# Performance work log

Measured on AMD Instinct MI355X. Metric: run time of the kernel, lower is better.

The kernel has to match this reference:

```python
import jax, jax.numpy as jnp
import numpy as np


def setup_inputs() -> dict:
    key = jax.random.key(0)
    k1, k2, k3 = jax.random.split(key, 3)
    n1, n2, L, n_S, sub_dim = 768, 768, 128, 30, 16
    X1 = jax.random.randint(k1, (n1, L), 0, n_S, dtype=jnp.int64)
    X2 = jax.random.randint(k2, (n2, L), 0, n_S, dtype=jnp.int64)
    a = jnp.ones((1,), dtype=jnp.float32)  # Parameter a=1.0
    A = jax.random.normal(k3, (n_S, sub_dim), dtype=jnp.float32)  # nn.init.normal_(A, 0, 1)
    w_vec = jnp.zeros((L * (L - 1) // 2,), dtype=jnp.float32)  # torch.zeros init
    return {"X1": X1, "X2": X2, "a": a, "A": A, "w_vec": w_vec}


def reference(X1, X2, a, A, w_vec):
    n1, L = X1.shape
    n2, _ = X2.shape
    # build symmetric soft weight matrix; diagonal stays sigmoid(0)=0.5 as in torch
    i_x, i_y = np.tril_indices(L, k=-1)
    W = jnp.zeros((L, L), dtype=w_vec.dtype)
    W = W.at[i_x, i_y].set(w_vec).at[i_y, i_x].set(w_vec)
    w = jax.nn.sigmoid(W)  # (L, L)

    S = A @ A.T  # (n_S, n_S) substitution matrix

    def wdk(subs):
        # quadratic form sum_{i,j} subs[...,i] * w[i,j] * subs[...,j]
        return jnp.sum((subs @ w) * subs, axis=-1)

    d1 = S[X1, X1]            # (n1, L) self-substitution scores
    d2 = S[X2, X2]            # (n2, L)
    k1 = wdk(d1)[:, None]     # (n1, 1)
    k2 = wdk(d2)[None, :]     # (1, n2)

    # cross pair gather: subs[a, b, l] = S[X1[a, l], X2[b, l]]  -> (n1, n2, L)
    subs = S[X1[:, None, :], X2[None, :, :]]
    K = wdk(subs)             # (n1, n2)

    K = K / jnp.sqrt(k1) / jnp.sqrt(k2)
    return a ** 2 * K
```

## Files before the change

kernel.cpp:

```cpp
#include <hip/hip_runtime.h>
#include <hip/hip_bf16.h>

typedef __attribute__((ext_vector_type(8))) short short8;
typedef __attribute__((ext_vector_type(4))) float f32x4;
typedef unsigned long long ull;

#define N1 768
#define N2 768
#define LL 128
#define NS 30

__device__ __forceinline__ unsigned short f2b(float f) {
  unsigned int u = __float_as_uint(f);
  unsigned int r = (u + 0x7fffu + ((u >> 16) & 1u)) >> 16;
  return (unsigned short)r;
}

__global__ void prep_kernel(const float* __restrict__ A, const float* __restrict__ w_vec,
                            float* __restrict__ wf, unsigned short* __restrict__ wb,
                            float* __restrict__ Sdiag, unsigned short* __restrict__ Sbg) {
  int b = blockIdx.x, t = threadIdx.x;
  if (b == 0) {
    for (int idx = t; idx < NS * NS; idx += 256) {
      int i = idx / NS, j = idx - i * NS;
      float acc = 0.f;
#pragma unroll
      for (int k = 0; k < 16; ++k) acc += A[i * 16 + k] * A[j * 16 + k];
      Sbg[i * 32 + j] = f2b(acc);
      if (i == j) Sdiag[i] = acc;
    }
  } else {
    int base = (b - 1) * 512;
#pragma unroll
    for (int k = 0; k < 2; ++k) {
      int idx = base + k * 256 + t;
      int l = idx >> 7, mm = idx & (LL - 1);
      float sig;
      if (l == mm) {
        sig = 0.5f;
      } else {
        int hi = l > mm ? l : mm, lo = l > mm ? mm : l;
        sig = 1.f / (1.f + expf(-w_vec[hi * (hi - 1) / 2 + lo]));
      }
      wf[idx] = sig;
      wb[idx] = f2b(sig);
    }
  }
}

__global__ __launch_bounds__(128) void norm_kernel(
    const int* __restrict__ X1, const int* __restrict__ X2,
    const float* __restrict__ Sdiag, const float* __restrict__ wf,
    float* __restrict__ inv1, float* __restrict__ inv2,
    const float* __restrict__ a_ptr) {
  __shared__ __align__(16) float d[8][LL];
  __shared__ float wsum[2][8];
  const int t = threadIdx.x;
  const int r0 = blockIdx.x * 8;
#pragma unroll
  for (int r = 0; r < 8; ++r) {
    int row = r0 + r;
    const int* X = (row < N1) ? (X1 + row * LL) : (X2 + (row - N1) * LL);
    d[r][t] = Sdiag[X[t]];
  }
  __syncthreads();
  const float4* w4 = reinterpret_cast<const float4*>(wf + t * LL);
  float s[8] = {0.f, 0.f, 0.f, 0.f, 0.f, 0.f, 0.f, 0.f};
#pragma unroll 8
  for (int q = 0; q < 32; ++q) {
    float4 wv = w4[q];
#pragma unroll
    for (int r = 0; r < 8; ++r) {
      float4 dd = *reinterpret_cast<const float4*>(&d[r][q * 4]);
      s[r] += wv.x * dd.x + wv.y * dd.y + wv.z * dd.z + wv.w * dd.w;
    }
  }
#pragma unroll
  for (int r = 0; r < 8; ++r) {
    float v = s[r] * d[r][t];
    v += __shfl_xor(v, 1);
    v += __shfl_xor(v, 2);
    v += __shfl_xor(v, 4);
    v += __shfl_xor(v, 8);
    v += __shfl_xor(v, 16);
    v += __shfl_xor(v, 32);
    if ((t & 63) == 0) wsum[t >> 6][r] = v;
  }
  __syncthreads();
  if (t < 8) {
    int row = r0 + t;
    float k = wsum[0][t] + wsum[1][t];
    if (row < N1) inv1[row] = a_ptr[0] * a_ptr[0] / sqrtf(k);
    else inv2[row - N1] = 1.f / sqrtf(k);
  }
}

__global__ __launch_bounds__(512, 4) void main_kernel(
    const int* __restrict__ X1, const int* __restrict__ X2,
    const unsigned short* __restrict__ wbg, const unsigned short* __restrict__ Sbg,
    const float* __restrict__ inv1, const float* __restrict__ inv2,
    float* __restrict__ out) {
  __shared__ __align__(16) unsigned short sV[256 * LL];
  __shared__ __align__(16) unsigned short sSb[960];
  __shared__ __align__(16) unsigned char x1B[16 * 144];
  __shared__ __align__(16) unsigned char x2B[16 * 144];
  __shared__ __align__(16) float red[4 * 256];

  const int t = threadIdx.x;
  const int lane = t & 63, wave = t >> 6;
  const int m = lane & 15, kg = lane >> 4;
  const int i0 = blockIdx.y * 16, j0 = blockIdx.x * 16;
  char* sVb = reinterpret_cast<char*>(sV);

  float iv1v = 0.f, iv2v = 0.f;
  if (t < 256) {
    iv1v = inv1[i0 + (t >> 4)];
    iv2v = inv2[j0 + (t & 15)];
  }

  if (t < 120) reinterpret_cast<uint4*>(sSb)[t] = reinterpret_cast<const uint4*>(Sbg)[t];

  if (t < 256) {
    int row = t >> 4, seg = t & 15;
    const int4* p1 = reinterpret_cast<const int4*>(X1 + (i0 + row) * LL + seg * 8);
    int4 a0 = p1[0], a1 = p1[1];
    ull v = 0;
    v |= (ull)(a0.x & 0xff);
    v |= (ull)(a0.y & 0xff) << 8;
    v |= (ull)(a0.z & 0xff) << 16;
    v |= (ull)(a0.w & 0xff) << 24;
    v |= (ull)(a1.x & 0xff) << 32;
    v |= (ull)(a1.y & 0xff) << 40;
    v |= (ull)(a1.z & 0xff) << 48;
    v |= (ull)(a1.w & 0xff) << 56;
    *reinterpret_cast<ull*>(x1B + row * 144 + seg * 8) = v;
    const int4* p2p = reinterpret_cast<const int4*>(X2 + (j0 + row) * LL + seg * 8);
    int4 b0 = p2p[0], b1 = p2p[1];
    ull u = 0;
    u |= (ull)(b0.x & 0xff);
    u |= (ull)(b0.y & 0xff) << 8;
    u |= (ull)(b0.z & 0xff) << 16;
    u |= (ull)(b0.w & 0xff) << 24;
    u |= (ull)(b1.x & 0xff) << 32;
    u |= (ull)(b1.y & 0xff) << 40;
    u |= (ull)(b1.z & 0xff) << 48;
    u |= (ull)(b1.w & 0xff) << 56;
    *reinterpret_cast<ull*>(x2B + row * 144 + seg * 8) = u;
  }
  __syncthreads();

  {
    const int p2 = t & 255;
    const int h2 = t >> 8;
    const char* a1p = reinterpret_cast<const char*>(x1B) + (p2 >> 4) * 144 + 64 * h2;
    const char* a2p = reinterpret_cast<const char*>(x2B) + (p2 & 15) * 144 + 64 * h2;
    uint4 A0 = *reinterpret_cast<const uint4*>(a1p);
    uint4 A1 = *reinterpret_cast<const uint4*>(a1p + 16);
    uint4 A2 = *reinterpret_cast<const uint4*>(a1p + 32);
    uint4 A3 = *reinterpret_cast<const uint4*>(a1p + 48);
    uint4 B0 = *reinterpret_cast<const uint4*>(a2p);
    uint4 B1 = *reinterpret_cast<const uint4*>(a2p + 16);
    uint4 B2 = *reinterpret_cast<const uint4*>(a2p + 32);
    uint4 B3 = *reinterpret_cast<const uint4*>(a2p + 48);
    const int swz = (p2 & 7) << 4;
    char* wbase = sVb + p2 * 256;
#define QUAD(u1, u2, w0, w1)                                                        \
    {                                                                               \
      unsigned a0_ = (u1) & 255u, a1_ = ((u1) >> 8) & 255u;                         \
      unsigned a2_ = ((u1) >> 16) & 255u, a3_ = (u1) >> 24;                         \
      unsigned b0_ = (u2) & 255u, b1_ = ((u2) >> 8) & 255u;                         \
      unsigned b2_ = ((u2) >> 16) & 255u, b3_ = (u2) >> 24;                         \
      unsigned g0 = sSb[(a0_ << 5) | b0_];                                          \
      unsigned g1 = sSb[(a1_ << 5) | b1_];                                          \
      unsigned g2 = sSb[(a2_ << 5) | b2_];                                          \
      unsigned g3 = sSb[(a3_ << 5) | b3_];                                          \
      w0 = g0 | (g1 << 16);                                                         \
      w1 = g2 | (g3 << 16);                                                         \
    }
#define OCT(o, U1a, U2a, U1b, U2b)                                                  \
    {                                                                               \
      uint4 pk;                                                                     \
      QUAD(U1a, U2a, pk.x, pk.y)                                                    \
      QUAD(U1b, U2b, pk.z, pk.w)                                                    \
      *reinterpret_cast<uint4*>(wbase + ((128 * h2 + 16 * (o)) ^ swz)) = pk;        \
    }
    OCT(0, A0.x, B0.x, A0.y, B0.y)
    OCT(1, A0.z, B0.z, A0.w, B0.w)
    OCT(2, A1.x, B1.x, A1.y, B1.y)
    OCT(3, A1.z, B1.z, A1.w, B1.w)
    OCT(4, A2.x, B2.x, A2.y, B2.y)
    OCT(5, A2.z, B2.z, A2.w, B2.w)
    OCT(6, A3.x, B3.x, A3.y, B3.y)
    OCT(7, A3.z, B3.z, A3.w, B3.w)
#undef OCT
#undef QUAD
  }

  const int lg = wave & 3, ph = wave >> 2;
  short8 wreg[2][4];
  {
    const char* wby = reinterpret_cast<const char*>(wbg);
#pragma unroll
    for (int lt = 0; lt < 2; ++lt)
#pragma unroll
      for (int kk = 0; kk < 4; ++kk)
        wreg[lt][kk] = *reinterpret_cast<const short8*>(
            wby + (lg * 32 + lt * 16 + m) * 256 + kk * 64 + kg * 16);
  }
  __syncthreads();

#pragma unroll
  for (int pt = 0; pt < 8; ++pt) {
    const int p = ph * 128 + pt * 16 + m;
    const int sw = (p & 7) << 4;
    const char* base = sVb + p * 256;
    short8 bv[4];
#pragma unroll
    for (int kk = 0; kk < 4; ++kk)
      bv[kk] = *reinterpret_cast<const short8*>(base + ((kk * 64 + kg * 16) ^ sw));
    f32x4 a0 = {0.f, 0.f, 0.f, 0.f}, a1 = {0.f, 0.f, 0.f, 0.f};
#pragma unroll
    for (int kk = 0; kk < 4; ++kk) {
      a0 = __builtin_amdgcn_mfma_f32_16x16x32_bf16(wreg[0][kk], bv[kk], a0, 0, 0, 0);
      a1 = __builtin_amdgcn_mfma_f32_16x16x32_bf16(wreg[1][kk], bv[kk], a1, 0, 0, 0);
    }
    float kp = 0.f;
    {
      uint2 vv = *reinterpret_cast<const uint2*>(base + ((64 * lg + 8 * kg) ^ sw));
      kp += a0[0] * __uint_as_float(vv.x << 16) + a0[1] * __uint_as_float(vv.x & 0xffff0000u) +
            a0[2] * __uint_as_float(vv.y << 16) + a0[3] * __uint_as_float(vv.y & 0xffff0000u);
    }
    {
      uint2 vv = *reinterpret_cast<const uint2*>(base + ((64 * lg + 32 + 8 * kg) ^ sw));
      kp += a1[0] * __uint_as_float(vv.x << 16) + a1[1] * __uint_as_float(vv.x & 0xffff0000u) +
            a1[2] * __uint_as_float(vv.y << 16) + a1[3] * __uint_as_float(vv.y & 0xffff0000u);
    }
    kp += __shfl_xor(kp, 16);
    kp += __shfl_xor(kp, 32);
    if (kg == 0) red[lg * 256 + p] = kp;
  }
  __syncthreads();

  if (t < 256) {
    float s = red[t] + red[256 + t] + red[512 + t] + red[768 + t];
    out[(i0 + (t >> 4)) * N2 + j0 + (t & 15)] = s * iv1v * iv2v;
  }
}

extern "C" void kernel_launch(void* const* d_in, const int* in_sizes, int n_in,
                              void* d_out, int out_size, void* d_ws, size_t ws_size,
                              hipStream_t stream) {
  const int* X1 = (const int*)d_in[0];
  const int* X2 = (const int*)d_in[1];
  const float* a = (const float*)d_in[2];
  const float* A = (const float*)d_in[3];
  const float* w_vec = (const float*)d_in[4];
  float* out = (float*)d_out;

  char* ws = (char*)d_ws;
  float* wf = (float*)(ws + 0);
  unsigned short* wb = (unsigned short*)(ws + 65536);
  float* Sdiag = (float*)(ws + 98304);
  unsigned short* Sbg = (unsigned short*)(ws + 98432);
  float* inv1 = (float*)(ws + 100352);
  float* inv2 = (float*)(ws + 103424);

  prep_kernel<<<33, 256, 0, stream>>>(A, w_vec, wf, wb, Sdiag, Sbg);
  norm_kernel<<<(N1 + N2) / 8, 128, 0, stream>>>(X1, X2, Sdiag, wf, inv1, inv2, a);
  main_kernel<<<dim3(N2 / 16, N1 / 16), 512, 0, stream>>>(X1, X2, wb, Sbg, inv1, inv2, out);
}
```

Before: 54.22 us.

## Split MFMA work across waves by 64-row W slices instead of 32

Re-partitions the per-block quadratic-form work so each wave owns 64 rows of W (four 16-row tiles) and half the pairs, instead of 32 rows and all 128-pair halves. Each B fragment loaded from LDS is reused across four MFMA chains instead of two, which halves the LDS B reads and the reduction buffer size. W fragments are now loaded with inline-asm global loads followed by an explicit wait. The cost is double the W register footprint (16 short8 per lane), which may pressure VGPRs under the 512x4 launch bound.

```diff
diff --git a/kernel.cpp b/kernel.cpp
--- a/kernel.cpp
+++ b/kernel.cpp
@@ -104,7 +104,7 @@
   __shared__ __align__(16) unsigned short sSb[960];
   __shared__ __align__(16) unsigned char x1B[16 * 144];
   __shared__ __align__(16) unsigned char x2B[16 * 144];
-  __shared__ __align__(16) float red[4 * 256];
+  __shared__ __align__(16) float red[2 * 256];
 
   const int t = threadIdx.x;
   const int lane = t & 63, wave = t >> 6;
@@ -196,53 +196,53 @@
 #undef QUAD
   }
 
-  const int lg = wave & 3, ph = wave >> 2;
-  short8 wreg[2][4];
+  const int lg2 = wave & 1, ph = wave >> 1;
+  short8 wreg[4][4];
   {
-    const char* wby = reinterpret_cast<const char*>(wbg);
-#pragma unroll
-    for (int lt = 0; lt < 2; ++lt)
-#pragma unroll
-      for (int kk = 0; kk < 4; ++kk)
-        wreg[lt][kk] = *reinterpret_cast<const short8*>(
-            wby + (lg * 32 + lt * 16 + m) * 256 + kk * 64 + kg * 16);
-  }
-  __syncthreads();
-
-#pragma unroll
-  for (int pt = 0; pt < 8; ++pt) {
-    const int p = ph * 128 + pt * 16 + m;
+    const char* wby = reinterpret_cast<const char*>(wbg) + (lg2 * 64 + m) * 256 + kg * 16;
+#pragma unroll
+    for (int lt = 0; lt < 4; ++lt)
+#pragma unroll
+      for (int kk = 0; kk < 4; ++kk) {
+        const char* addr = wby + lt * 16 * 256 + kk * 64;
+        asm volatile("global_load_dwordx4 %0, %1, off"
+                     : "=v"(wreg[lt][kk])
+                     : "v"(addr));
+      }
+    asm volatile("s_waitcnt vmcnt(0)" ::: "memory");
+    __builtin_amdgcn_sched_barrier(0);
+  }
+  __syncthreads();
+
+#pragma unroll
+  for (int pt = 0; pt < 4; ++pt) {
+    const int p = ph * 64 + pt * 16 + m;
     const int sw = (p & 7) << 4;
     const char* base = sVb + p * 256;
     short8 bv[4];
 #pragma unroll
     for (int kk = 0; kk < 4; ++kk)
       bv[kk] = *reinterpret_cast<const short8*>(base + ((kk * 64 + kg * 16) ^ sw));
-    f32x4 a0 = {0.f, 0.f, 0.f, 0.f}, a1 = {0.f, 0.f, 0.f, 0.f};
-#pragma unroll
-    for (int kk = 0; kk < 4; ++kk) {
-      a0 = __builtin_amdgcn_mfma_f32_16x16x32_bf16(wreg[0][kk], bv[kk], a0, 0, 0, 0);
-      a1 = __builtin_amdgcn_mfma_f32_16x16x32_bf16(wreg[1][kk], bv[kk], a1, 0, 0, 0);
-    }
     float kp = 0.f;
-    {
-      uint2 vv = *reinterpret_cast<const uint2*>(base + ((64 * lg + 8 * kg) ^ sw));
-      kp += a0[0] * __uint_as_float(vv.x << 16) + a0[1] * __uint_as_float(vv.x & 0xffff0000u) +
-            a0[2] * __uint_as_float(vv.y << 16) + a0[3] * __uint_as_float(vv.y & 0xffff0000u);
-    }
-    {
-      uint2 vv = *reinterpret_cast<const uint2*>(base + ((64 * lg + 32 + 8 * kg) ^ sw));
-      kp += a1[0] * __uint_as_float(vv.x << 16) + a1[1] * __uint_as_float(vv.x & 0xffff0000u) +
-            a1[2] * __uint_as_float(vv.y << 16) + a1[3] * __uint_as_float(vv.y & 0xffff0000u);
+#pragma unroll
+    for (int lt = 0; lt < 4; ++lt) {
+      f32x4 acc = {0.f, 0.f, 0.f, 0.f};
+#pragma unroll
+      for (int kk = 0; kk < 4; ++kk)
+        acc = __builtin_amdgcn_mfma_f32_16x16x32_bf16(wreg[lt][kk], bv[kk], acc, 0, 0, 0);
+      uint2 vv = *reinterpret_cast<const uint2*>(
+          base + ((128 * lg2 + 32 * lt + 8 * kg) ^ sw));
+      kp += acc[0] * __uint_as_float(vv.x << 16) + acc[1] * __uint_as_float(vv.x & 0xffff0000u) +
+            acc[2] * __uint_as_float(vv.y << 16) + acc[3] * __uint_as_float(vv.y & 0xffff0000u);
     }
     kp += __shfl_xor(kp, 16);
     kp += __shfl_xor(kp, 32);
-    if (kg == 0) red[lg * 256 + p] = kp;
+    if (kg == 0) red[lg2 * 256 + p] = kp;
   }
   __syncthreads();
 
   if (t < 256) {
-    float s = red[t] + red[256 + t] + red[512 + t] + red[768 + t];
+    float s = red[t] + red[256 + t];
     out[(i0 + (t >> 4)) * N2 + j0 + (t & 15)] = s * iv1v * iv2v;
   }
 }
```

After: 73.63 us. +35.8%, slower.

## Merge prep and norm kernels into one launch, rebuild weights per block

Applied to the files above, without the earlier changes.

The separate prep and norm kernels are folded into a single aux kernel. The first 33 blocks write the bf16 weights and substitution matrix, and the remaining 192 blocks each recompute the sigmoid weight matrix and the self-substitution diagonal in shared memory to get the norms. This removes one kernel launch and the dependency between them, at the cost of redundant sigmoid and exp work per block and a serial loop of up to 127 iterations per thread with an unbalanced triangular workload. It also raises the wave priority around the MFMA loop in the main kernel.

```diff
diff --git a/kernel.cpp b/kernel.cpp
--- a/kernel.cpp
+++ b/kernel.cpp
@@ -16,80 +16,104 @@
   return (unsigned short)r;
 }
 
-__global__ void prep_kernel(const float* __restrict__ A, const float* __restrict__ w_vec,
-                            float* __restrict__ wf, unsigned short* __restrict__ wb,
-                            float* __restrict__ Sdiag, unsigned short* __restrict__ Sbg) {
-  int b = blockIdx.x, t = threadIdx.x;
-  if (b == 0) {
-    for (int idx = t; idx < NS * NS; idx += 256) {
-      int i = idx / NS, j = idx - i * NS;
-      float acc = 0.f;
-#pragma unroll
-      for (int k = 0; k < 16; ++k) acc += A[i * 16 + k] * A[j * 16 + k];
-      Sbg[i * 32 + j] = f2b(acc);
-      if (i == j) Sdiag[i] = acc;
-    }
-  } else {
-    int base = (b - 1) * 512;
-#pragma unroll
-    for (int k = 0; k < 2; ++k) {
-      int idx = base + k * 256 + t;
-      int l = idx >> 7, mm = idx & (LL - 1);
-      float sig;
-      if (l == mm) {
-        sig = 0.5f;
-      } else {
-        int hi = l > mm ? l : mm, lo = l > mm ? mm : l;
-        sig = 1.f / (1.f + expf(-w_vec[hi * (hi - 1) / 2 + lo]));
+__global__ __launch_bounds__(256) void aux_kernel(
+    const int* __restrict__ X1, const int* __restrict__ X2,
+    const float* __restrict__ A, const float* __restrict__ w_vec,
+    const float* __restrict__ a_ptr, unsigned short* __restrict__ wb,
+    unsigned short* __restrict__ Sbg, float* __restrict__ inv1,
+    float* __restrict__ inv2) {
+  __shared__ __align__(16) float wfull[128][132];
+  __shared__ __align__(16) float d[8][132];
+  __shared__ float sdg[32];
+  __shared__ float wsum[4][4];
+
+  const int b = blockIdx.x, t = threadIdx.x;
+
+  if (b < 33) {
+    if (b == 0) {
+      for (int idx = t; idx < NS * NS; idx += 256) {
+        int i = idx / NS, j = idx - i * NS;
+        float acc = 0.f;
+#pragma unroll
+        for (int k = 0; k < 16; ++k) acc += A[i * 16 + k] * A[j * 16 + k];
+        Sbg[i * 32 + j] = f2b(acc);
       }
-      wf[idx] = sig;
-      wb[idx] = f2b(sig);
-    }
-  }
-}
-
-__global__ __launch_bounds__(128) void norm_kernel(
-    const int* __restrict__ X1, const int* __restrict__ X2,
-    const float* __restrict__ Sdiag, const float* __restrict__ wf,
-    float* __restrict__ inv1, float* __restrict__ inv2,
-    const float* __restrict__ a_ptr) {
-  __shared__ __align__(16) float d[8][LL];
-  __shared__ float wsum[2][8];
-  const int t = threadIdx.x;
-  const int r0 = blockIdx.x * 8;
-#pragma unroll
-  for (int r = 0; r < 8; ++r) {
-    int row = r0 + r;
-    const int* X = (row < N1) ? (X1 + row * LL) : (X2 + (row - N1) * LL);
-    d[r][t] = Sdiag[X[t]];
-  }
-  __syncthreads();
-  const float4* w4 = reinterpret_cast<const float4*>(wf + t * LL);
-  float s[8] = {0.f, 0.f, 0.f, 0.f, 0.f, 0.f, 0.f, 0.f};
+    } else {
+      int base = (b - 1) * 512;
+#pragma unroll
+      for (int k = 0; k < 2; ++k) {
+        int idx = base + k * 256 + t;
+        int l = idx >> 7, mm = idx & (LL - 1);
+        float sig;
+        if (l == mm) {
+          sig = 0.5f;
+        } else {
+          int hi = l > mm ? l : mm, lo = l > mm ? mm : l;
+          sig = 1.f / (1.f + expf(-w_vec[hi * (hi - 1) / 2 + lo]));
+        }
+        wb[idx] = f2b(sig);
+      }
+    }
+    return;
+  }
+
+  const int r0 = (b - 33) * 8;
+  const int wave = t >> 6, h = t >> 7, tl = t & 127, lane = t & 63;
+
+  if (t < NS) {
+    float acc = 0.f;
+#pragma unroll
+    for (int c = 0; c < 16; ++c) { float v = A[t * 16 + c]; acc += v * v; }
+    sdg[t] = acc;
+  }
+  if (t < 128) {
+    const float* src = w_vec + t * (t - 1) / 2;
+    wfull[t][t] = 0.5f;
+    for (int mm = 0; mm < t; ++mm) {
+      float sig = 1.f / (1.f + expf(-src[mm]));
+      wfull[t][mm] = sig;
+      wfull[mm][t] = sig;
+    }
+  }
+  __syncthreads();
+
+  if (t < 128) {
+#pragma unroll
+    for (int r = 0; r < 8; ++r) {
+      int row = r0 + r;
+      const int* X = (row < N1) ? (X1 + row * LL) : (X2 + (row - N1) * LL);
+      d[r][t] = sdg[X[t]];
+    }
+  }
+  __syncthreads();
+
+  const float4* w4 = reinterpret_cast<const float4*>(&wfull[tl][0]);
+  float s[4] = {0.f, 0.f, 0.f, 0.f};
 #pragma unroll 8
   for (int q = 0; q < 32; ++q) {
     float4 wv = w4[q];
 #pragma unroll
-    for (int r = 0; r < 8; ++r) {
-      float4 dd = *reinterpret_cast<const float4*>(&d[r][q * 4]);
+    for (int r = 0; r < 4; ++r) {
+      float4 dd = *reinterpret_cast<const float4*>(&d[h * 4 + r][q * 4]);
       s[r] += wv.x * dd.x + wv.y * dd.y + wv.z * dd.z + wv.w * dd.w;
     }
   }
 #pragma unroll
-  for (int r = 0; r < 8; ++r) {
-    float v = s[r] * d[r][t];
+  for (int r = 0; r < 4; ++r) {
+    float v = s[r] * d[h * 4 + r][tl];
     v += __shfl_xor(v, 1);
     v += __shfl_xor(v, 2);
     v += __shfl_xor(v, 4);
     v += __shfl_xor(v, 8);
     v += __shfl_xor(v, 16);
     v += __shfl_xor(v, 32);
-    if ((t & 63) == 0) wsum[t >> 6][r] = v;
+    if (lane == 0) wsum[wave][r] = v;
   }
   __syncthreads();
   if (t < 8) {
+    int hh = t >> 2, r = t & 3;
+    float k = wsum[hh * 2][r] + wsum[hh * 2 + 1][r];
     int row = r0 + t;
-    float k = wsum[0][t] + wsum[1][t];
     if (row < N1) inv1[row] = a_ptr[0] * a_ptr[0] / sqrtf(k);
     else inv2[row - N1] = 1.f / sqrtf(k);
   }
@@ -209,6 +233,7 @@
   }
   __syncthreads();
 
+  __builtin_amdgcn_s_setprio(1);
 #pragma unroll
   for (int pt = 0; pt < 8; ++pt) {
     const int p = ph * 128 + pt * 16 + m;
@@ -239,6 +264,7 @@
     kp += __shfl_xor(kp, 32);
     if (kg == 0) red[lg * 256 + p] = kp;
   }
+  __builtin_amdgcn_s_setprio(0);
   __syncthreads();
 
   if (t < 256) {
@@ -258,14 +284,11 @@
   float* out = (float*)d_out;
 
   char* ws = (char*)d_ws;
-  float* wf = (float*)(ws + 0);
-  unsigned short* wb = (unsigned short*)(ws + 65536);
-  float* Sdiag = (float*)(ws + 98304);
-  unsigned short* Sbg = (unsigned short*)(ws + 98432);
-  float* inv1 = (float*)(ws + 100352);
-  float* inv2 = (float*)(ws + 103424);
-
-  prep_kernel<<<33, 256, 0, stream>>>(A, w_vec, wf, wb, Sdiag, Sbg);
-  norm_kernel<<<(N1 + N2) / 8, 128, 0, stream>>>(X1, X2, Sdiag, wf, inv1, inv2, a);
+  unsigned short* wb = (unsigned short*)(ws + 0);
+  unsigned short* Sbg = (unsigned short*)(ws + 32768);
+  float* inv1 = (float*)(ws + 36864);
+  float* inv2 = (float*)(ws + 39936);
+
+  aux_kernel<<<225, 256, 0, stream>>>(X1, X2, A, w_vec, a, wb, Sbg, inv1, inv2);
   main_kernel<<<dim3(N2 / 16, N1 / 16), 512, 0, stream>>>(X1, X2, wb, Sbg, inv1, inv2, out);
 }
```

After: 55.83 us. 3.0% more time.
